# Optimization experiments

Hardware: AMD Instinct MI355X
Metric: run time of the kernel (lower is better)

## Reference

```python
import jax, jax.numpy as jnp
import numpy as np

B, D, H, DM, O = 8192, 512, 1024, 2048, 256


def setup_inputs() -> dict:
    key = jax.random.key(0)
    ks = jax.random.split(key, 24)
    def rn(k, shape, scale=1.0):
        return jax.random.normal(k, shape, dtype=jnp.float32) * scale
    w = 0.02  # weight init scale
    return {
        "x":  rn(ks[0], (B, D)),
        "h0": rn(ks[1], (B, H), 0.1), "h1": rn(ks[2], (B, H), 0.1),
        "c0": rn(ks[3], (B, H), 0.1), "c1": rn(ks[4], (B, H), 0.1),
        # Bernoulli keep masks with model_prob=1.0 -> all ones
        "m0": jnp.ones((B, H), jnp.float32), "m1": jnp.ones((B, H), jnp.float32),
        # layer 0 gate weights: in = D + H = 1536
        "Wf0": rn(ks[5], (D + H, H), w), "bf0": jnp.full((H,), 0.01, jnp.float32),
        "Wi0": rn(ks[6], (D + H, H), w), "bi0": jnp.full((H,), 0.01, jnp.float32),
        "Wc0": rn(ks[7], (D + H, H), w), "bc0": jnp.full((H,), 0.01, jnp.float32),
        "Wo0": rn(ks[8], (D + H, H), w), "bo0": jnp.full((H,), 0.01, jnp.float32),
        # layer 1 gate weights: in = H + H = 2048
        "Wf1": rn(ks[9],  (2 * H, H), w), "bf1": jnp.full((H,), 0.01, jnp.float32),
        "Wi1": rn(ks[10], (2 * H, H), w), "bi1": jnp.full((H,), 0.01, jnp.float32),
        "Wc1": rn(ks[11], (2 * H, H), w), "bc1": jnp.full((H,), 0.01, jnp.float32),
        "Wo1": rn(ks[12], (2 * H, H), w), "bo1": jnp.full((H,), 0.01, jnp.float32),
        # output MLP: H -> DM -> O (identity activation per default nn.Sequential())
        "Wm1": rn(ks[13], (H, DM), w), "bm1": jnp.full((DM,), 0.01, jnp.float32),
        "Wm2": rn(ks[14], (DM, O), w), "bm2": jnp.full((O,), 0.01, jnp.float32),
    }


def _lstm_cell(comb, c, Wf, bf, Wi, bi, Wc, bc, Wo, bo):
    # fuse the 4 gate GEMMs into one matmul, then split
    W = jnp.concatenate([Wf, Wi, Wc, Wo], axis=1)      # [in, 4H]
    b = jnp.concatenate([bf, bi, bc, bo])               # [4H]
    g = comb @ W + b                                    # [B, 4H]
    f, i, ct, o = jnp.split(g, 4, axis=1)
    c_new = jax.nn.sigmoid(f) * c + jax.nn.sigmoid(i) * jnp.tanh(ct)
    h_new = jax.nn.sigmoid(o) * jnp.tanh(c_new)
    return h_new, c_new


def reference(x, h0, h1, c0, c1, m0, m1,
              Wf0, bf0, Wi0, bi0, Wc0, bc0, Wo0, bo0,
              Wf1, bf1, Wi1, bi1, Wc1, bc1, Wo1, bo1,
              Wm1, bm1, Wm2, bm2):
    # layer 0: combined = cat(input, h0 * mask0)
    comb0 = jnp.concatenate([x, h0 * m0], axis=1)       # [B, D+H]
    h0n, c0n = _lstm_cell(comb0, c0, Wf0, bf0, Wi0, bi0, Wc0, bc0, Wo0, bo0)
    # layer 1: combined = cat(h0_new * mask0, h1 * mask1)
    comb1 = jnp.concatenate([h0n * m0, h1 * m1], axis=1)  # [B, 2H]
    h1n, c1n = _lstm_cell(comb1, c1, Wf1, bf1, Wi1, bi1, Wc1, bc1, Wo1, bo1)
    # output MLP (dropout p=0 is identity; activation is identity Sequential)
    out = (h1n @ Wm1 + bm1) @ Wm2 + bm2                 # [B, O]
    return out, h0n, h1n, c0n, c1n
```

## Files before the change

### kernel.cpp

```cpp
#include <hip/hip_runtime.h>
#include <hip/hip_bf16.h>
#include <cstdint>
#include <cstddef>

#define DI __device__ __forceinline__

typedef __attribute__((ext_vector_type(8))) short short8;
typedef __attribute__((ext_vector_type(4))) float f32x4;

static constexpr int Bb = 8192, Dd = 512, Hh = 1024;

DI short f2b(float f) {
  union { __hip_bfloat16 h; short s; } u;
  u.h = __float2bfloat16(f);
  return u.s;
}

DI float sigm(float x) {
  float e = __builtin_amdgcn_exp2f(-1.4426950408889634f * x);
  return __builtin_amdgcn_rcpf(1.0f + e);
}
DI float tanh_(float x) {
  float xc = fminf(fmaxf(x, -20.0f), 20.0f);
  float e = __builtin_amdgcn_exp2f(-2.8853900817779268f * xc);
  return (1.0f - e) * __builtin_amdgcn_rcpf(1.0f + e);
}

DI void gload16(const void* g, void* l) {
  __builtin_amdgcn_global_load_lds(
      (const __attribute__((address_space(1))) uint32_t*)g,
      (__attribute__((address_space(3))) uint32_t*)l, 16, 0, 0);
}


__global__ void conv_A0(const float* __restrict__ x, const float* __restrict__ h0,
                        const float* __restrict__ m0, short* __restrict__ A0) {
  const int row = blockIdx.x, t = threadIdx.x;
  float v[8];
  if (t < 64) {
    const float4* p = (const float4*)(x + (size_t)row * Dd + t * 8);
    float4 a = p[0], b = p[1];
    v[0] = a.x; v[1] = a.y; v[2] = a.z; v[3] = a.w;
    v[4] = b.x; v[5] = b.y; v[6] = b.z; v[7] = b.w;
  } else {
    const int j = t * 8 - 512;
    const float4* ph = (const float4*)(h0 + (size_t)row * Hh + j);
    const float4* pm = (const float4*)(m0 + (size_t)row * Hh + j);
    float4 a = ph[0], b = ph[1], ma = pm[0], mb = pm[1];
    v[0] = a.x * ma.x; v[1] = a.y * ma.y; v[2] = a.z * ma.z; v[3] = a.w * ma.w;
    v[4] = b.x * mb.x; v[5] = b.y * mb.y; v[6] = b.z * mb.z; v[7] = b.w * mb.w;
  }
  short8 o;
  #pragma unroll
  for (int q = 0; q < 8; q++) o[q] = f2b(v[q]);
  *(short8*)(A0 + (size_t)row * 1536 + t * 8) = o;
}

__global__ void conv_A1hi(const float* __restrict__ h1, const float* __restrict__ m1,
                          short* __restrict__ A1) {
  const int row = blockIdx.x, t = threadIdx.x;
  const int j = t * 8;
  const float4* ph = (const float4*)(h1 + (size_t)row * Hh + j);
  const float4* pm = (const float4*)(m1 + (size_t)row * Hh + j);
  float4 a = ph[0], b = ph[1], ma = pm[0], mb = pm[1];
  float v[8] = {a.x * ma.x, a.y * ma.y, a.z * ma.z, a.w * ma.w,
                b.x * mb.x, b.y * mb.y, b.z * mb.z, b.w * mb.w};
  short8 o;
  #pragma unroll
  for (int q = 0; q < 8; q++) o[q] = f2b(v[q]);
  *(short8*)(A1 + (size_t)row * 2048 + 1024 + j) = o;
}

__global__ void transpose_conv4(const float* __restrict__ s0, const float* __restrict__ s1,
                                const float* __restrict__ s2, const float* __restrict__ s3,
                                short* __restrict__ dst, int N, int K) {
  __shared__ float t[64][65];
  const int g = blockIdx.z;
  const float* src = (g == 0) ? s0 : (g == 1) ? s1 : (g == 2) ? s2 : s3;
  const int k0 = blockIdx.x * 64, n0 = blockIdx.y * 64;
  const int tid = threadIdx.x;
  const int r = tid >> 2, c0 = (tid & 3) * 16;
  const float* s = src + (size_t)(k0 + r) * N + n0 + c0;
  #pragma unroll
  for (int q = 0; q < 16; q += 4) {
    float4 v = *(const float4*)(s + q);
    t[r][c0 + q + 0] = v.x; t[r][c0 + q + 1] = v.y;
    t[r][c0 + q + 2] = v.z; t[r][c0 + q + 3] = v.w;
  }
  __syncthreads();
  const int n = n0 + r;
  const int j = (n >> 4) * 64 + g * 16 + (n & 15);
  short8 o0, o1;
  #pragma unroll
  for (int q = 0; q < 8; q++) o0[q] = f2b(t[c0 + q][r]);
  #pragma unroll
  for (int q = 0; q < 8; q++) o1[q] = f2b(t[c0 + 8 + q][r]);
  short* d = dst + (size_t)j * K + k0 + c0;
  *(short8*)d = o0;
  *((short8*)d + 1) = o1;
}

__global__ void transpose_conv(const float* __restrict__ src, short* __restrict__ dst,
                               int N, int K) {
  __shared__ float t[64][65];
  const int k0 = blockIdx.x * 64, n0 = blockIdx.y * 64;
  const int tid = threadIdx.x;
  const int r = tid >> 2, c0 = (tid & 3) * 16;
  const float* s = src + (size_t)(k0 + r) * N + n0 + c0;
  #pragma unroll
  for (int q = 0; q < 16; q += 4) {
    float4 v = *(const float4*)(s + q);
    t[r][c0 + q + 0] = v.x; t[r][c0 + q + 1] = v.y;
    t[r][c0 + q + 2] = v.z; t[r][c0 + q + 3] = v.w;
  }
  __syncthreads();
  const int n = n0 + r;
  short8 o0, o1;
  #pragma unroll
  for (int q = 0; q < 8; q++) o0[q] = f2b(t[c0 + q][r]);
  #pragma unroll
  for (int q = 0; q < 8; q++) o1[q] = f2b(t[c0 + 8 + q][r]);
  short* d = dst + (size_t)n * K + k0 + c0;
  *(short8*)d = o0;
  *((short8*)d + 1) = o1;
}

__global__ void conv_plain(const float* __restrict__ src, short* __restrict__ dst, int n8) {
  const int id = blockIdx.x * blockDim.x + threadIdx.x;
  if (id >= n8) return;
  const float4* p = (const float4*)(src + (size_t)id * 8);
  float4 a = p[0], b = p[1];
  short8 o;
  o[0] = f2b(a.x); o[1] = f2b(a.y); o[2] = f2b(a.z); o[3] = f2b(a.w);
  o[4] = f2b(b.x); o[5] = f2b(b.y); o[6] = f2b(b.z); o[7] = f2b(b.w);
  *(short8*)(dst + (size_t)id * 8) = o;
}

__global__ void bp_init(const float* __restrict__ bm2, float* __restrict__ bp) {
  bp[threadIdx.x] = bm2[threadIdx.x];
}
__global__ void bp_acc(const float* __restrict__ bm1, const float* __restrict__ Wm2,
                       float* __restrict__ bp) {
  const int o = threadIdx.x;
  const int k0 = blockIdx.x * 64;
  float s = 0.f;
  #pragma unroll 4
  for (int k = 0; k < 64; k++) s += bm1[k0 + k] * Wm2[(size_t)(k0 + k) * 256 + o];
  atomicAdd(&bp[o], s);
}

template <int EPI>
__global__ __launch_bounds__(256) void gemm_bt(
    const short* __restrict__ A, const short* __restrict__ Bt, int K,
    short* __restrict__ Cb, int ldc,
    float* __restrict__ outp, const float* __restrict__ bpv) {
  __shared__ __align__(16) short sA[128 * 32];
  __shared__ __align__(16) short sB[128 * 32];
  const int tid = threadIdx.x;
  const int lane = tid & 63;
  const int wave = tid >> 6;
  const int wm = wave >> 1, wn = wave & 1;
  const int bm = blockIdx.x, bn = blockIdx.y;
  const int lr = lane & 15, lq = lane >> 4;

  f32x4 acc[4][4] = {};

  const short* pA = A + ((size_t)(bm * 128 + (tid >> 2))) * K + (tid & 3) * 8;
  const short* pB = Bt + ((size_t)(bn * 128 + (tid >> 2))) * K + (tid & 3) * 8;
  short* lA = sA + tid * 8;
  short* lB = sB + tid * 8;
  const int aoff = (wm * 64 + lr) * 32 + lq * 8;
  const int boff = (wn * 64 + lr) * 32 + lq * 8;

  for (int k0 = 0; k0 < K; k0 += 32) {
    gload16(pA + k0, lA);
    gload16(pA + (size_t)64 * K + k0, lA + 2048);
    gload16(pB + k0, lB);
    gload16(pB + (size_t)64 * K + k0, lB + 2048);
    __syncthreads();
    short8 af[4], bv[4];
    #pragma unroll
    for (int m = 0; m < 4; m++) af[m] = *(const short8*)&sA[aoff + m * 512];
    #pragma unroll
    for (int n = 0; n < 4; n++) bv[n] = *(const short8*)&sB[boff + n * 512];
    #pragma unroll
    for (int m = 0; m < 4; m++)
      #pragma unroll
      for (int n = 0; n < 4; n++)
        acc[m][n] = __builtin_amdgcn_mfma_f32_16x16x32_bf16(af[m], bv[n], acc[m][n], 0, 0, 0);
    __syncthreads();
  }

  const int crow0 = bm * 128 + wm * 64 + lq * 4;
  const int ccol0 = bn * 128 + wn * 64 + lr;

  if constexpr (EPI == 0) {
    #pragma unroll
    for (int m = 0; m < 4; m++)
      #pragma unroll
      for (int r = 0; r < 4; r++) {
        const int row = crow0 + m * 16 + r;
        #pragma unroll
        for (int n = 0; n < 4; n++)
          Cb[(size_t)row * ldc + ccol0 + n * 16] = f2b(acc[m][n][r]);
      }
  } else {
    float bvv[4];
    #pragma unroll
    for (int n = 0; n < 4; n++) bvv[n] = bpv[ccol0 + n * 16];
    #pragma unroll
    for (int m = 0; m < 4; m++)
      #pragma unroll
      for (int r = 0; r < 4; r++) {
        const int row = crow0 + m * 16 + r;
        #pragma unroll
        for (int n = 0; n < 4; n++)
          outp[(size_t)row * 256 + ccol0 + n * 16] = acc[m][n][r] + bvv[n];
      }
  }
}


#define STA(buf, h, kt) { const short* s_ = gA + (size_t)(h) * 64 * K + (size_t)(kt) * 64; \
    gload16(s_ + aS0, &sA[buf][h][tid * 8]);                                               \
    gload16(s_ + aS1, &sA[buf][h][4096 + tid * 8]); }
#define STB(buf, h, kt) { const short* s_ = gB + (size_t)(h) * 128 * K + (size_t)(kt) * 64; \
    gload16(s_ + bS0, &sB[buf][h][tid * 8]);                                                \
    gload16(s_ + bS1, &sB[buf][h][4096 + tid * 8]); }

#define LDB(buf) {                                                \
    const short* bb = &sB[buf][bh][brb];                          \
    _Pragma("unroll") for (int n = 0; n < 4; n++) {               \
      bv[n][0] = *(const short8*)(bb + n * 1024 + sw0);           \
      bv[n][1] = *(const short8*)(bb + n * 1024 + sw1); } }

#define LDA_(buf, q, av) {                                        \
    const short* ab = &sA[buf][(q) >> 1][arb + ((q) & 1) * 2048]; \
    av[0][0] = *(const short8*)(ab + sw0);                        \
    av[0][1] = *(const short8*)(ab + sw1);                        \
    av[1][0] = *(const short8*)(ab + 1024 + sw0);                 \
    av[1][1] = *(const short8*)(ab + 1024 + sw1); }

#define MM(q, av) {                                               \
    __builtin_amdgcn_s_setprio(1);                                \
    _Pragma("unroll") for (int m = 0; m < 2; m++)                 \
    _Pragma("unroll") for (int n = 0; n < 4; n++) {               \
      acc[2*(q)+m][n] = __builtin_amdgcn_mfma_f32_16x16x32_bf16(av[m][0], bv[n][0], acc[2*(q)+m][n], 0, 0, 0); \
      acc[2*(q)+m][n] = __builtin_amdgcn_mfma_f32_16x16x32_bf16(av[m][1], bv[n][1], acc[2*(q)+m][n], 0, 0, 0); } \
    __builtin_amdgcn_s_setprio(0); }

#define BARR() __builtin_amdgcn_s_barrier()
#define VM6()  asm volatile("s_waitcnt vmcnt(6)")
#define LG8()  asm volatile("s_waitcnt lgkmcnt(8)")
#define LG0()  asm volatile("s_waitcnt lgkmcnt(0)")

#define PH(buf, q, STG, vm) { short8 av[2][2]; LDA_(buf, q, av); STG; \
    if (vm) VM6(); BARR(); LG0(); MM(q, av); BARR(); }

__global__ __launch_bounds__(512, 2) void gemm8_lstm(
    const short* __restrict__ A, const short* __restrict__ Bt, const int K,
    const float* __restrict__ cprev, float* __restrict__ hout,
    float* __restrict__ cout, short* __restrict__ anext, const int ldan,
    const float* __restrict__ mask,
    const float* __restrict__ bF, const float* __restrict__ bI,
    const float* __restrict__ bC, const float* __restrict__ bO) {
  __shared__ __align__(16) short sA[2][2][8192];
  __shared__ __align__(16) short sB[2][2][8192];
  const int tid = threadIdx.x;
  const int lane = tid & 63, wid = tid >> 6;
  const int wr = wid >> 2, wc = wid & 3;
  const int lr = lane & 15, lq = lane >> 4;
  const int bm = blockIdx.x, bn = blockIdx.y;

  const int NT = K >> 6;
  const int NIT = NT >> 1;

  const int r0 = tid >> 3;
  const int csw = (tid & 7) ^ (r0 & 7);
  const int growA0 = ((r0 >> 5) & 1) * 32 + (r0 & 31);
  const int growA1 = 128 + growA0;
  const size_t aS0 = (size_t)growA0 * K + csw * 8;
  const size_t aS1 = (size_t)growA1 * K + csw * 8;
  const size_t bS0 = (size_t)r0 * K + csw * 8;
  const size_t bS1 = (size_t)(r0 + 64) * K + csw * 8;
  const short* gA = A + (size_t)bm * 256 * K;
  const short* gB = Bt + (size_t)bn * 256 * K;

  const int arb = (wr * 64 + lr) * 64;
  const int brb = ((wc & 1) * 64 + lr) * 64;
  const int bh = wc >> 1;
  const int sw0 = ((lq) ^ (lr & 7)) * 8;
  const int sw1 = ((4 + lq) ^ (lr & 7)) * 8;

  f32x4 acc[8][4] = {};
  short8 bv[4][2];

  STB(0, 0, 0); STB(0, 1, 0); STA(0, 0, 0); STA(0, 1, 0);
  STB(1, 0, 1); STB(1, 1, 1); STA(1, 0, 1);
  VM6(); BARR();

  for (int it = 0; it < NIT; ++it) {
    const int k1 = 2 * it + 1;
    int t2 = 2 * it + 2; if (t2 >= NT) t2 = 0;
    int t3 = 2 * it + 3; if (t3 >= NT) t3 = 1;
    { short8 av[2][2]; LDB(0); LDA_(0, 0, av); STA(1, 1, k1);
      LG8(); BARR(); LG0(); MM(0, av); BARR(); }
    PH(0, 1, STB(0, 0, t2), 0);
    PH(0, 2, STB(0, 1, t2), 0);
    PH(0, 3, STA(0, 0, t2), 1);
    { short8 av[2][2]; LDB(1); LDA_(1, 0, av); STA(0, 1, t2);
      LG8(); BARR(); LG0(); MM(0, av); BARR(); }
    PH(1, 1, STB(1, 0, t3), 0);
    PH(1, 2, STB(1, 1, t3), 0);
    PH(1, 3, STA(1, 0, t3), 1);
  }

  const int n = (bn * 4 + wc) * 16 + lr;
  const float bf_ = bF[n], bi_ = bI[n], bc_ = bC[n], bo_ = bO[n];
  const int row0 = bm * 256 + wr * 128 + lq * 4;

  float cp[4], mk[4], cpn[4], mkn[4];
  #pragma unroll
  for (int rr = 0; rr < 4; rr++) {
    const size_t idx = (size_t)(row0 + rr) * 1024 + n;
    cp[rr] = cprev[idx];
    mk[rr] = mask ? mask[idx] : 1.0f;
  }
  #pragma unroll
  for (int mf = 0; mf < 8; mf++) {
    if (mf < 7) {
      #pragma unroll
      for (int rr = 0; rr < 4; rr++) {
        const size_t idx2 = (size_t)(row0 + (mf + 1) * 16 + rr) * 1024 + n;
        cpn[rr] = cprev[idx2];
        mkn[rr] = mask ? mask[idx2] : 1.0f;
      }
    }
    #pragma unroll
    for (int rr = 0; rr < 4; rr++) {
      const int row = row0 + mf * 16 + rr;
      const size_t idx = (size_t)row * 1024 + n;
      const float fg = sigm(acc[mf][0][rr] + bf_);
      const float ig = sigm(acc[mf][1][rr] + bi_);
      const float cg = tanh_(acc[mf][2][rr] + bc_);
      const float og = sigm(acc[mf][3][rr] + bo_);
      const float cn = fg * cp[rr] + ig * cg;
      const float hn = og * tanh_(cn);
      cout[idx] = cn;
      hout[idx] = hn;
      anext[(size_t)row * ldan + n] = f2b(hn * mk[rr]);
    }
    #pragma unroll
    for (int rr = 0; rr < 4; rr++) { cp[rr] = cpn[rr]; mk[rr] = mkn[rr]; }
  }
}


extern "C" void kernel_launch(void* const* d_in, const int* in_sizes, int n_in,
                              void* d_out, int out_size, void* d_ws, size_t ws_size,
                              hipStream_t stream) {
  (void)in_sizes; (void)n_in; (void)out_size; (void)ws_size;
  const float* x   = (const float*)d_in[0];
  const float* h0  = (const float*)d_in[1];
  const float* h1  = (const float*)d_in[2];
  const float* c0  = (const float*)d_in[3];
  const float* c1  = (const float*)d_in[4];
  const float* m0  = (const float*)d_in[5];
  const float* m1  = (const float*)d_in[6];
  const float* Wf0 = (const float*)d_in[7];  const float* bf0 = (const float*)d_in[8];
  const float* Wi0 = (const float*)d_in[9];  const float* bi0 = (const float*)d_in[10];
  const float* Wc0 = (const float*)d_in[11]; const float* bc0 = (const float*)d_in[12];
  const float* Wo0 = (const float*)d_in[13]; const float* bo0 = (const float*)d_in[14];
  const float* Wf1 = (const float*)d_in[15]; const float* bf1 = (const float*)d_in[16];
  const float* Wi1 = (const float*)d_in[17]; const float* bi1 = (const float*)d_in[18];
  const float* Wc1 = (const float*)d_in[19]; const float* bc1 = (const float*)d_in[20];
  const float* Wo1 = (const float*)d_in[21]; const float* bo1 = (const float*)d_in[22];
  const float* Wm1 = (const float*)d_in[23]; const float* bm1 = (const float*)d_in[24];
  const float* Wm2 = (const float*)d_in[25]; const float* bm2 = (const float*)d_in[26];

  float* dout  = (float*)d_out;
  float* out_o = dout;
  float* h0n   = dout + 2097152;
  float* h1n   = h0n + 8388608;
  float* c0n   = h1n + 8388608;
  float* c1n   = c0n + 8388608;

  char* ws = (char*)d_ws;
  short* A0   = (short*)(ws);
  short* A1   = (short*)(ws + 25165824);
  short* A2   = (short*)(ws + 58720256);
  short* WT0  = (short*)(ws + 75497472);
  short* WT1  = (short*)(ws + 88080384);
  short* Wm1b = (short*)(ws + 104857600);
  short* Wm2T = (short*)(ws + 109051904);
  short* WpT  = (short*)(ws + 110100480);
  float* bp   = (float*)(ws + 110624768);

  conv_A0<<<dim3(8192), dim3(192), 0, stream>>>(x, h0, m0, A0);
  conv_A1hi<<<dim3(8192), dim3(128), 0, stream>>>(h1, m1, A1);
  transpose_conv4<<<dim3(24, 16, 4), dim3(256), 0, stream>>>(Wf0, Wi0, Wc0, Wo0, WT0, 1024, 1536);
  transpose_conv4<<<dim3(32, 16, 4), dim3(256), 0, stream>>>(Wf1, Wi1, Wc1, Wo1, WT1, 1024, 2048);
  conv_plain<<<dim3(1024), dim3(256), 0, stream>>>(Wm1, Wm1b, 262144);
  transpose_conv<<<dim3(32, 4), dim3(256), 0, stream>>>(Wm2, Wm2T, 256, 2048);
  bp_init<<<dim3(1), dim3(256), 0, stream>>>(bm2, bp);
  bp_acc<<<dim3(32), dim3(256), 0, stream>>>(bm1, Wm2, bp);

  gemm_bt<0><<<dim3(2, 8), dim3(256), 0, stream>>>(
      Wm2T, Wm1b, 2048, WpT, 1024, nullptr, nullptr);

  gemm8_lstm<<<dim3(32, 16), dim3(512), 0, stream>>>(
      A0, WT0, 1536, c0, h0n, c0n, A1, 2048, m0, bf0, bi0, bc0, bo0);

  gemm8_lstm<<<dim3(32, 16), dim3(512), 0, stream>>>(
      A1, WT1, 2048, c1, h1n, c1n, A2, 1024, nullptr, bf1, bi1, bc1, bo1);

  gemm_bt<1><<<dim3(64, 2), dim3(256), 0, stream>>>(
      A2, WpT, 1024, nullptr, 0, out_o, bp);
}
```

Baseline: 393.6 us.

## Process two N-tiles per LSTM GEMM block, overlapping epilogue with next B prefetch

Each gemm8_lstm block now computes two consecutive 256-column N tiles, halving the grid to 32x8 blocks. After the first main loop it issues the B-tile loads for the second tile and only then runs the first epilogue, so the epilogue's global traffic overlaps the prefetch. The loop relies on the A stages already sitting in LDS from the wraparound prefetch. The two activation-conversion kernels are merged into one launch. The risks are fewer blocks to fill the CUs (256 blocks), a longer serial path per block, and subtle dependence on what the buffers hold after the loop.

```diff
diff --git a/kernel.cpp b/kernel.cpp
--- a/kernel.cpp
+++ b/kernel.cpp
@@ -33,42 +33,42 @@
 }
 
 
-__global__ void conv_A0(const float* __restrict__ x, const float* __restrict__ h0,
-                        const float* __restrict__ m0, short* __restrict__ A0) {
+__global__ void conv_acts(const float* __restrict__ x, const float* __restrict__ h0,
+                          const float* __restrict__ m0, const float* __restrict__ h1,
+                          const float* __restrict__ m1,
+                          short* __restrict__ A0, short* __restrict__ A1) {
   const int row = blockIdx.x, t = threadIdx.x;
   float v[8];
-  if (t < 64) {
-    const float4* p = (const float4*)(x + (size_t)row * Dd + t * 8);
-    float4 a = p[0], b = p[1];
-    v[0] = a.x; v[1] = a.y; v[2] = a.z; v[3] = a.w;
-    v[4] = b.x; v[5] = b.y; v[6] = b.z; v[7] = b.w;
+  if (t < 192) {
+    if (t < 64) {
+      const float4* p = (const float4*)(x + (size_t)row * Dd + t * 8);
+      float4 a = p[0], b = p[1];
+      v[0] = a.x; v[1] = a.y; v[2] = a.z; v[3] = a.w;
+      v[4] = b.x; v[5] = b.y; v[6] = b.z; v[7] = b.w;
+    } else {
+      const int j = t * 8 - 512;
+      const float4* ph = (const float4*)(h0 + (size_t)row * Hh + j);
+      const float4* pm = (const float4*)(m0 + (size_t)row * Hh + j);
+      float4 a = ph[0], b = ph[1], ma = pm[0], mb = pm[1];
+      v[0] = a.x * ma.x; v[1] = a.y * ma.y; v[2] = a.z * ma.z; v[3] = a.w * ma.w;
+      v[4] = b.x * mb.x; v[5] = b.y * mb.y; v[6] = b.z * mb.z; v[7] = b.w * mb.w;
+    }
+    short8 o;
+    #pragma unroll
+    for (int q = 0; q < 8; q++) o[q] = f2b(v[q]);
+    *(short8*)(A0 + (size_t)row * 1536 + t * 8) = o;
   } else {
-    const int j = t * 8 - 512;
-    const float4* ph = (const float4*)(h0 + (size_t)row * Hh + j);
-    const float4* pm = (const float4*)(m0 + (size_t)row * Hh + j);
+    const int j = (t - 192) * 8;
+    const float4* ph = (const float4*)(h1 + (size_t)row * Hh + j);
+    const float4* pm = (const float4*)(m1 + (size_t)row * Hh + j);
     float4 a = ph[0], b = ph[1], ma = pm[0], mb = pm[1];
     v[0] = a.x * ma.x; v[1] = a.y * ma.y; v[2] = a.z * ma.z; v[3] = a.w * ma.w;
     v[4] = b.x * mb.x; v[5] = b.y * mb.y; v[6] = b.z * mb.z; v[7] = b.w * mb.w;
-  }
-  short8 o;
-  #pragma unroll
-  for (int q = 0; q < 8; q++) o[q] = f2b(v[q]);
-  *(short8*)(A0 + (size_t)row * 1536 + t * 8) = o;
-}
-
-__global__ void conv_A1hi(const float* __restrict__ h1, const float* __restrict__ m1,
-                          short* __restrict__ A1) {
-  const int row = blockIdx.x, t = threadIdx.x;
-  const int j = t * 8;
-  const float4* ph = (const float4*)(h1 + (size_t)row * Hh + j);
-  const float4* pm = (const float4*)(m1 + (size_t)row * Hh + j);
-  float4 a = ph[0], b = ph[1], ma = pm[0], mb = pm[1];
-  float v[8] = {a.x * ma.x, a.y * ma.y, a.z * ma.z, a.w * ma.w,
-                b.x * mb.x, b.y * mb.y, b.z * mb.z, b.w * mb.w};
-  short8 o;
-  #pragma unroll
-  for (int q = 0; q < 8; q++) o[q] = f2b(v[q]);
-  *(short8*)(A1 + (size_t)row * 2048 + 1024 + j) = o;
+    short8 o;
+    #pragma unroll
+    for (int q = 0; q < 8; q++) o[q] = f2b(v[q]);
+    *(short8*)(A1 + (size_t)row * 2048 + 1024 + j) = o;
+  }
 }
 
 __global__ void transpose_conv4(const float* __restrict__ s0, const float* __restrict__ s1,
@@ -257,6 +257,63 @@
 #define PH(buf, q, STG, vm) { short8 av[2][2]; LDA_(buf, q, av); STG; \
     if (vm) VM6(); BARR(); LG0(); MM(q, av); BARR(); }
 
+#define MAINLOOP()                                                        \
+  for (int it = 0; it < NIT; ++it) {                                      \
+    const int k1 = 2 * it + 1;                                            \
+    int t2 = 2 * it + 2; if (t2 >= NT) t2 = 0;                            \
+    int t3 = 2 * it + 3; if (t3 >= NT) t3 = 1;                            \
+    { short8 av[2][2]; LDB(0); LDA_(0, 0, av); STA(1, 1, k1);             \
+      LG8(); BARR(); LG0(); MM(0, av); BARR(); }                          \
+    PH(0, 1, STB(0, 0, t2), 0);                                           \
+    PH(0, 2, STB(0, 1, t2), 0);                                           \
+    PH(0, 3, STA(0, 0, t2), 1);                                           \
+    { short8 av[2][2]; LDB(1); LDA_(1, 0, av); STA(0, 1, t2);             \
+      LG8(); BARR(); LG0(); MM(0, av); BARR(); }                          \
+    PH(1, 1, STB(1, 0, t3), 0);                                           \
+    PH(1, 2, STB(1, 1, t3), 0);                                           \
+    PH(1, 3, STA(1, 0, t3), 1);                                           \
+  }
+
+#define EPILOG(bn_e) {                                                    \
+  const int n = ((bn_e) * 4 + wc) * 16 + lr;                              \
+  const float bf_ = bF[n], bi_ = bI[n], bc_ = bC[n], bo_ = bO[n];         \
+  const int row0 = bm * 256 + wr * 128 + lq * 4;                          \
+  float cp[4], mk[4], cpn[4], mkn[4];                                     \
+  _Pragma("unroll")                                                       \
+  for (int rr = 0; rr < 4; rr++) {                                        \
+    const size_t idx = (size_t)(row0 + rr) * 1024 + n;                    \
+    cp[rr] = cprev[idx];                                                  \
+    mk[rr] = mask ? mask[idx] : 1.0f;                                     \
+  }                                                                       \
+  _Pragma("unroll")                                                       \
+  for (int mf = 0; mf < 8; mf++) {                                        \
+    if (mf < 7) {                                                         \
+      _Pragma("unroll")                                                   \
+      for (int rr = 0; rr < 4; rr++) {                                    \
+        const size_t idx2 = (size_t)(row0 + (mf + 1) * 16 + rr) * 1024 + n; \
+        cpn[rr] = cprev[idx2];                                            \
+        mkn[rr] = mask ? mask[idx2] : 1.0f;                               \
+      }                                                                   \
+    }                                                                     \
+    _Pragma("unroll")                                                     \
+    for (int rr = 0; rr < 4; rr++) {                                      \
+      const int row = row0 + mf * 16 + rr;                                \
+      const size_t idx = (size_t)row * 1024 + n;                          \
+      const float fg = sigm(acc[mf][0][rr] + bf_);                        \
+      const float ig = sigm(acc[mf][1][rr] + bi_);                        \
+      const float cg = tanh_(acc[mf][2][rr] + bc_);                       \
+      const float og = sigm(acc[mf][3][rr] + bo_);                        \
+      const float cn = fg * cp[rr] + ig * cg;                             \
+      const float hn = og * tanh_(cn);                                    \
+      cout[idx] = cn;                                                     \
+      hout[idx] = hn;                                                     \
+      anext[(size_t)row * ldan + n] = f2b(hn * mk[rr]);                   \
+    }                                                                     \
+    _Pragma("unroll")                                                     \
+    for (int rr = 0; rr < 4; rr++) { cp[rr] = cpn[rr]; mk[rr] = mkn[rr]; } \
+  }                                                                       \
+}
+
 __global__ __launch_bounds__(512, 2) void gemm8_lstm(
     const short* __restrict__ A, const short* __restrict__ Bt, const int K,
     const float* __restrict__ cprev, float* __restrict__ hout,
@@ -270,7 +327,8 @@
   const int lane = tid & 63, wid = tid >> 6;
   const int wr = wid >> 2, wc = wid & 3;
   const int lr = lane & 15, lq = lane >> 4;
-  const int bm = blockIdx.x, bn = blockIdx.y;
+  const int bm = blockIdx.x;
+  const int bn0 = blockIdx.y * 2;
 
   const int NT = K >> 6;
   const int NIT = NT >> 1;
@@ -284,7 +342,7 @@
   const size_t bS0 = (size_t)r0 * K + csw * 8;
   const size_t bS1 = (size_t)(r0 + 64) * K + csw * 8;
   const short* gA = A + (size_t)bm * 256 * K;
-  const short* gB = Bt + (size_t)bn * 256 * K;
+  const short* gB = Bt + (size_t)bn0 * 256 * K;
 
   const int arb = (wr * 64 + lr) * 64;
   const int brb = ((wc & 1) * 64 + lr) * 64;
@@ -299,60 +357,27 @@
   STB(1, 0, 1); STB(1, 1, 1); STA(1, 0, 1);
   VM6(); BARR();
 
-  for (int it = 0; it < NIT; ++it) {
-    const int k1 = 2 * it + 1;
-    int t2 = 2 * it + 2; if (t2 >= NT) t2 = 0;
-    int t3 = 2 * it + 3; if (t3 >= NT) t3 = 1;
-    { short8 av[2][2]; LDB(0); LDA_(0, 0, av); STA(1, 1, k1);
-      LG8(); BARR(); LG0(); MM(0, av); BARR(); }
-    PH(0, 1, STB(0, 0, t2), 0);
-    PH(0, 2, STB(0, 1, t2), 0);
-    PH(0, 3, STA(0, 0, t2), 1);
-    { short8 av[2][2]; LDB(1); LDA_(1, 0, av); STA(0, 1, t2);
-      LG8(); BARR(); LG0(); MM(0, av); BARR(); }
-    PH(1, 1, STB(1, 0, t3), 0);
-    PH(1, 2, STB(1, 1, t3), 0);
-    PH(1, 3, STA(1, 0, t3), 1);
-  }
-
-  const int n = (bn * 4 + wc) * 16 + lr;
-  const float bf_ = bF[n], bi_ = bI[n], bc_ = bC[n], bo_ = bO[n];
-  const int row0 = bm * 256 + wr * 128 + lq * 4;
-
-  float cp[4], mk[4], cpn[4], mkn[4];
-  #pragma unroll
-  for (int rr = 0; rr < 4; rr++) {
-    const size_t idx = (size_t)(row0 + rr) * 1024 + n;
-    cp[rr] = cprev[idx];
-    mk[rr] = mask ? mask[idx] : 1.0f;
-  }
-  #pragma unroll
-  for (int mf = 0; mf < 8; mf++) {
-    if (mf < 7) {
-      #pragma unroll
-      for (int rr = 0; rr < 4; rr++) {
-        const size_t idx2 = (size_t)(row0 + (mf + 1) * 16 + rr) * 1024 + n;
-        cpn[rr] = cprev[idx2];
-        mkn[rr] = mask ? mask[idx2] : 1.0f;
-      }
-    }
-    #pragma unroll
-    for (int rr = 0; rr < 4; rr++) {
-      const int row = row0 + mf * 16 + rr;
-      const size_t idx = (size_t)row * 1024 + n;
-      const float fg = sigm(acc[mf][0][rr] + bf_);
-      const float ig = sigm(acc[mf][1][rr] + bi_);
-      const float cg = tanh_(acc[mf][2][rr] + bc_);
-      const float og = sigm(acc[mf][3][rr] + bo_);
-      const float cn = fg * cp[rr] + ig * cg;
-      const float hn = og * tanh_(cn);
-      cout[idx] = cn;
-      hout[idx] = hn;
-      anext[(size_t)row * ldan + n] = f2b(hn * mk[rr]);
-    }
-    #pragma unroll
-    for (int rr = 0; rr < 4; rr++) { cp[rr] = cpn[rr]; mk[rr] = mkn[rr]; }
-  }
+  MAINLOOP();
+
+  asm volatile("s_waitcnt vmcnt(0)");
+  BARR();
+  gB = Bt + (size_t)(bn0 + 1) * 256 * K;
+  STB(0, 0, 0); STB(0, 1, 0); STB(1, 0, 1); STB(1, 1, 1);
+
+  EPILOG(bn0);
+
+  #pragma unroll
+  for (int mf = 0; mf < 8; mf++)
+    #pragma unroll
+    for (int nn = 0; nn < 4; nn++)
+      acc[mf][nn] = (f32x4){0.f, 0.f, 0.f, 0.f};
+
+  asm volatile("s_waitcnt vmcnt(4)");
+  BARR();
+
+  MAINLOOP();
+
+  EPILOG(bn0 + 1);
 }
 
 
@@ -396,8 +421,7 @@
   short* WpT  = (short*)(ws + 110100480);
   float* bp   = (float*)(ws + 110624768);
 
-  conv_A0<<<dim3(8192), dim3(192), 0, stream>>>(x, h0, m0, A0);
-  conv_A1hi<<<dim3(8192), dim3(128), 0, stream>>>(h1, m1, A1);
+  conv_acts<<<dim3(8192), dim3(320), 0, stream>>>(x, h0, m0, h1, m1, A0, A1);
   transpose_conv4<<<dim3(24, 16, 4), dim3(256), 0, stream>>>(Wf0, Wi0, Wc0, Wo0, WT0, 1024, 1536);
   transpose_conv4<<<dim3(32, 16, 4), dim3(256), 0, stream>>>(Wf1, Wi1, Wc1, Wo1, WT1, 1024, 2048);
   conv_plain<<<dim3(1024), dim3(256), 0, stream>>>(Wm1, Wm1b, 262144);
@@ -408,10 +432,10 @@
   gemm_bt<0><<<dim3(2, 8), dim3(256), 0, stream>>>(
       Wm2T, Wm1b, 2048, WpT, 1024, nullptr, nullptr);
 
-  gemm8_lstm<<<dim3(32, 16), dim3(512), 0, stream>>>(
+  gemm8_lstm<<<dim3(32, 8), dim3(512), 0, stream>>>(
       A0, WT0, 1536, c0, h0n, c0n, A1, 2048, m0, bf0, bi0, bc0, bo0);
 
-  gemm8_lstm<<<dim3(32, 16), dim3(512), 0, stream>>>(
+  gemm8_lstm<<<dim3(32, 8), dim3(512), 0, stream>>>(
       A1, WT1, 2048, c1, h1n, c1n, A2, 1024, nullptr, bf1, bi1, bc1, bo1);
 
   gemm_bt<1><<<dim3(64, 2), dim3(256), 0, stream>>>(
```

After: 417.9 us. +6.2%, slower.
